# Kernel optimization log

Measured on AMD Instinct MI355X. Metric: run time of the kernel, lower is better.

Reference implementation:

```python
import jax, jax.numpy as jnp
import numpy as np

N = 12000       # nodes (Hi-C bins, max_num_nodes)
F_IN = 16       # number_genomic_annotations
HID = 4 * F_IN  # conv1 out = 64
NCLUST = 100    # n_clust
E = 384000      # edges (avg degree 32)


def setup_inputs() -> dict:
    key = jax.random.key(0)
    ks = jax.random.split(key, 8)
    x = jax.random.normal(ks[0], (N, F_IN), dtype=jnp.float32)
    edge_index = jax.random.randint(ks[1], (2, E), 0, N)
    edge_attr = jax.random.uniform(ks[2], (E,), dtype=jnp.float32)
    s1 = 1.0 / np.sqrt(F_IN)
    W1_rel = jax.random.uniform(ks[3], (HID, F_IN), minval=-s1, maxval=s1, dtype=jnp.float32)
    W1_root = jax.random.uniform(ks[4], (HID, F_IN), minval=-s1, maxval=s1, dtype=jnp.float32)
    b1 = jnp.zeros((HID,), jnp.float32)
    s2 = 1.0 / np.sqrt(HID)
    W2_rel = jax.random.uniform(ks[5], (NCLUST, HID), minval=-s2, maxval=s2, dtype=jnp.float32)
    W2_root = jax.random.uniform(ks[6], (NCLUST, HID), minval=-s2, maxval=s2, dtype=jnp.float32)
    b2 = jnp.zeros((NCLUST,), jnp.float32)
    return dict(x=x, edge_index=edge_index, edge_attr=edge_attr,
                W1_rel=W1_rel, W1_root=W1_root, b1=b1,
                W2_rel=W2_rel, W2_root=W2_root, b2=b2)


def _graph_conv(x, src, dst, ew, W_rel, W_root, b):
    # PyG GraphConv (aggr='add'): out = lin_rel(sum_j e_ji * x_j) + lin_root(x)
    msg = x[src] * ew[:, None]                       # [E, F]
    aggr = jax.ops.segment_sum(msg, dst, num_segments=N)  # [N, F]
    return aggr @ W_rel.T + b + x @ W_root.T


def reference(x, edge_index, edge_attr, W1_rel, W1_root, b1, W2_rel, W2_root, b2):
    src, dst = edge_index[0], edge_index[1]
    h = _graph_conv(x, src, dst, edge_attr, W1_rel, W1_root, b1)
    h = jax.nn.relu(h)  # dropout is identity in eval mode
    s_out = _graph_conv(h, src, dst, edge_attr, W2_rel, W2_root, b2)  # [N, NCLUST]

    # to_dense_adj (duplicate edges summed)
    adj = jnp.zeros((N, N), x.dtype).at[src, dst].add(edge_attr)  # [N, N]

    # dense_mincut_pool with S = x (as in the original forward), k = F_IN
    s_mc = jax.nn.softmax(x, axis=-1)      # [N, F_IN]
    as_ = adj @ s_mc                        # [N, F_IN]
    out_adj = s_mc.T @ as_                  # [F_IN, F_IN]
    mincut_num = jnp.trace(out_adj)
    d_flat = adj.sum(-1)                    # [N] degree
    mincut_den = jnp.einsum('ik,i,ik->', s_mc, d_flat, s_mc)  # trace(S^T D S)
    mc = -(mincut_num / mincut_den)

    ss = s_mc.T @ s_mc                      # [F_IN, F_IN]
    i_k = jnp.eye(F_IN, dtype=ss.dtype)
    o = jnp.linalg.norm(ss / jnp.linalg.norm(ss) - i_k / jnp.linalg.norm(i_k))

    return jax.nn.softmax(s_out, axis=-1), mc, o
```

## Files before the change

### kernel.cpp

```cpp
#include <hip/hip_runtime.h>
#include <math.h>

#define N_NODES 12000
#define F_INN 16
#define HIDD 64
#define NCLUST 100
#define NEDGE 384000
#define NBLK_N 47
#define CAP 96
#define EPT 4
#define NTHR_E (NEDGE / EPT)
#define NBLK_E (NTHR_E / 256)

#define OFF_COUNT   0
#define OFF_SCAL    12000
#define ZERO_ELEMS  12002
#define OFF_SSPART  12004
#define OFF_NORM2   24036
#define OFF_W2TREL  36036
#define OFF_W2TROOT 42436
#define OFF_SMC     48836
#define OFF_H       240836
#define OFF_SRCW    1008836

__global__ void zero_kernel(int* __restrict__ ws) {
    int i = blockIdx.x * 256 + threadIdx.x;
    if (i < ZERO_ELEMS) ws[i] = 0;
}

__global__ void phase0_kernel(const float* __restrict__ x, const int* __restrict__ ei,
                              const float* __restrict__ ew, float* __restrict__ smc,
                              float* __restrict__ norm2, int* __restrict__ count,
                              int2* __restrict__ srcw, const float* __restrict__ W2_rel,
                              const float* __restrict__ W2_root, float* __restrict__ w2t_rel,
                              float* __restrict__ w2t_root) {
    __shared__ float fl[6400];
    int t = threadIdx.x;
    int b = blockIdx.x;
    if (b < NBLK_N) {
        int i = b * 256 + t;
        if (i >= N_NODES) return;
        const float4* xr = (const float4*)(x + i * 16);
        float4 r0 = xr[0], r1 = xr[1], r2 = xr[2], r3 = xr[3];
        float v[16] = {r0.x, r0.y, r0.z, r0.w, r1.x, r1.y, r1.z, r1.w,
                       r2.x, r2.y, r2.z, r2.w, r3.x, r3.y, r3.z, r3.w};
        float m = v[0];
#pragma unroll
        for (int k = 1; k < 16; ++k) m = fmaxf(m, v[k]);
        float s = 0.f;
#pragma unroll
        for (int k = 0; k < 16; ++k) { v[k] = __expf(v[k] - m); s += v[k]; }
        float inv = 1.f / s;
        float n2 = 0.f;
#pragma unroll
        for (int k = 0; k < 16; ++k) { v[k] *= inv; n2 += v[k] * v[k]; }
        float4* so = (float4*)(smc + i * 16);
        so[0] = make_float4(v[0], v[1], v[2], v[3]);
        so[1] = make_float4(v[4], v[5], v[6], v[7]);
        so[2] = make_float4(v[8], v[9], v[10], v[11]);
        so[3] = make_float4(v[12], v[13], v[14], v[15]);
        norm2[i] = n2;
    } else if (b < NBLK_N + NBLK_E) {
        int tid = (b - NBLK_N) * 256 + t;
        int e0 = tid * EPT;
        int4 sv = *(const int4*)(ei + e0);
        int4 dv = *(const int4*)(ei + NEDGE + e0);
        float4 wv = *(const float4*)(ew + e0);
        int s[EPT] = {sv.x, sv.y, sv.z, sv.w};
        int d[EPT] = {dv.x, dv.y, dv.z, dv.w};
        float w[EPT] = {wv.x, wv.y, wv.z, wv.w};
        int pos[EPT];
#pragma unroll
        for (int i = 0; i < EPT; ++i) pos[i] = atomicAdd(&count[d[i]], 1);
#pragma unroll
        for (int i = 0; i < EPT; ++i)
            srcw[d[i] * CAP + pos[i]] = make_int2(s[i], __float_as_int(w[i]));
    } else {
        const float* src = (b == NBLK_N + NBLK_E) ? W2_rel : W2_root;
        float* dst = (b == NBLK_N + NBLK_E) ? w2t_rel : w2t_root;
        for (int i = t; i < 6400; i += 256) fl[i] = src[i];
        __syncthreads();
        for (int j = t; j < 6400; j += 256) {
            int kk = j / 100, cl = j - kk * 100;
            dst[j] = fl[cl * 64 + kk];
        }
    }
}

__global__ void pass2_kernel(const float* __restrict__ smc, float* __restrict__ sspart,
                             const int* __restrict__ ei, const float* __restrict__ ew,
                             const float* __restrict__ norm2, float* __restrict__ scal) {
    int t = threadIdx.x;
    int b = blockIdx.x;
    if (b < NBLK_N) {
        __shared__ float rows[256 * 17];
        int n = b * 256 + t;
        float* rp = rows + t * 17;
        if (n < N_NODES) {
            const float4* sr = (const float4*)(smc + n * 16);
            float4 a0 = sr[0], a1 = sr[1], a2 = sr[2], a3 = sr[3];
            rp[0] = a0.x;  rp[1] = a0.y;  rp[2] = a0.z;  rp[3] = a0.w;
            rp[4] = a1.x;  rp[5] = a1.y;  rp[6] = a1.z;  rp[7] = a1.w;
            rp[8] = a2.x;  rp[9] = a2.y;  rp[10] = a2.z; rp[11] = a2.w;
            rp[12] = a3.x; rp[13] = a3.y; rp[14] = a3.z; rp[15] = a3.w;
        } else {
#pragma unroll
            for (int k = 0; k < 16; ++k) rp[k] = 0.f;
        }
        __syncthreads();
        int a = t & 15, bb = t >> 4;
        float acc = 0.f;
#pragma unroll 4
        for (int r = 0; r < 256; ++r)
            acc = fmaf(rows[r * 17 + a], rows[r * 17 + bb], acc);
        sspart[b * 256 + t] = acc;
    } else {
        int tid = (b - NBLK_N) * 256 + t;
        int e0 = tid * EPT;
        int4 sv = *(const int4*)(ei + e0);
        int4 dv = *(const int4*)(ei + NEDGE + e0);
        float4 wv = *(const float4*)(ew + e0);
        int s[EPT] = {sv.x, sv.y, sv.z, sv.w};
        int d[EPT] = {dv.x, dv.y, dv.z, dv.w};
        float w[EPT] = {wv.x, wv.y, wv.z, wv.w};
        float np = 0.f, dp = 0.f;
#pragma unroll
        for (int i = 0; i < EPT; ++i) {
            const float4* ps = (const float4*)(smc + s[i] * 16);
            const float4* pd = (const float4*)(smc + d[i] * 16);
            float4 s0 = ps[0], s1 = ps[1], s2 = ps[2], s3 = ps[3];
            float4 d0 = pd[0], d1 = pd[1], d2 = pd[2], d3 = pd[3];
            float dot = s0.x * d0.x + s0.y * d0.y + s0.z * d0.z + s0.w * d0.w +
                        s1.x * d1.x + s1.y * d1.y + s1.z * d1.z + s1.w * d1.w +
                        s2.x * d2.x + s2.y * d2.y + s2.z * d2.z + s2.w * d2.w +
                        s3.x * d3.x + s3.y * d3.y + s3.z * d3.z + s3.w * d3.w;
            np = fmaf(w[i], dot, np);
            dp = fmaf(w[i], norm2[s[i]], dp);
        }
        __shared__ float redn[256], redd[256];
        redn[t] = np;
        redd[t] = dp;
        __syncthreads();
        for (int s2 = 128; s2 > 0; s2 >>= 1) {
            if (t < s2) { redn[t] += redn[t + s2]; redd[t] += redd[t + s2]; }
            __syncthreads();
        }
        if (t == 0) {
            atomicAdd(&scal[0], redn[0]);
            atomicAdd(&scal[1], redd[0]);
        }
    }
}

__global__ void fused1_kernel(const float* __restrict__ x, const int2* __restrict__ srcw,
                              const int* __restrict__ count, const float* __restrict__ W1_rel,
                              const float* __restrict__ W1_root, const float* __restrict__ b1,
                              float* __restrict__ h) {
    __shared__ float wrelT[16 * 64], wrootT[16 * 64], b1s[64];
    __shared__ float aggr[4][16], xs[4][16];
    int t = threadIdx.x;
    for (int idx = t; idx < 1024; idx += 256) {
        int f = idx >> 4, k = idx & 15;
        wrelT[(k << 6) + f] = W1_rel[idx];
        wrootT[(k << 6) + f] = W1_root[idx];
    }
    if (t < 64) b1s[t] = b1[t];
    int w = t >> 6, lane = t & 63;
    int n = blockIdx.x * 4 + w;
    int j = lane >> 4, c = lane & 15;
    int len = count[n];
    const int2* bucket = srcw + n * CAP;
    float acc = 0.f;
    int k = j;
    for (; k + 12 < len; k += 16) {
        int2 p0 = bucket[k], p1 = bucket[k + 4], p2 = bucket[k + 8], p3 = bucket[k + 12];
        float v0 = x[p0.x * 16 + c], v1 = x[p1.x * 16 + c];
        float v2 = x[p2.x * 16 + c], v3 = x[p3.x * 16 + c];
        acc = fmaf(v0, __int_as_float(p0.y), acc);
        acc = fmaf(v1, __int_as_float(p1.y), acc);
        acc = fmaf(v2, __int_as_float(p2.y), acc);
        acc = fmaf(v3, __int_as_float(p3.y), acc);
    }
    for (; k < len; k += 4) {
        int2 p = bucket[k];
        acc = fmaf(x[p.x * 16 + c], __int_as_float(p.y), acc);
    }
    acc += __shfl_down(acc, 32);
    acc += __shfl_down(acc, 16);
    if (lane < 16) { aggr[w][lane] = acc; xs[w][lane] = x[n * 16 + lane]; }
    __syncthreads();
    float o = b1s[lane];
#pragma unroll
    for (int kk = 0; kk < 16; ++kk)
        o = fmaf(aggr[w][kk], wrelT[(kk << 6) + lane],
                 fmaf(xs[w][kk], wrootT[(kk << 6) + lane], o));
    h[n * 64 + lane] = fmaxf(o, 0.f);
}

__global__ void fused2_kernel(const float* __restrict__ h, const int2* __restrict__ srcw,
                              const int* __restrict__ count, const float* __restrict__ w2t_rel,
                              const float* __restrict__ w2t_root, const float* __restrict__ b2,
                              float* __restrict__ out) {
    __shared__ float a2[4][64], hrow[4][64];
    __shared__ float logits[4][104];
    int t = threadIdx.x;
    int nn = t >> 6;
    int c = t & 63;
    int n = blockIdx.x * 4 + nn;
    int len = count[n];
    const int2* bucket = srcw + n * CAP;
    float acc = 0.f;
    int k = 0;
    for (; k + 7 < len; k += 8) {
        int2 p0 = bucket[k],     p1 = bucket[k + 1], p2 = bucket[k + 2], p3 = bucket[k + 3];
        int2 p4 = bucket[k + 4], p5 = bucket[k + 5], p6 = bucket[k + 6], p7 = bucket[k + 7];
        float v0 = h[p0.x * 64 + c], v1 = h[p1.x * 64 + c];
        float v2 = h[p2.x * 64 + c], v3 = h[p3.x * 64 + c];
        float v4 = h[p4.x * 64 + c], v5 = h[p5.x * 64 + c];
        float v6 = h[p6.x * 64 + c], v7 = h[p7.x * 64 + c];
        acc = fmaf(v0, __int_as_float(p0.y), acc);
        acc = fmaf(v1, __int_as_float(p1.y), acc);
        acc = fmaf(v2, __int_as_float(p2.y), acc);
        acc = fmaf(v3, __int_as_float(p3.y), acc);
        acc = fmaf(v4, __int_as_float(p4.y), acc);
        acc = fmaf(v5, __int_as_float(p5.y), acc);
        acc = fmaf(v6, __int_as_float(p6.y), acc);
        acc = fmaf(v7, __int_as_float(p7.y), acc);
    }
    for (; k < len; ++k) {
        int2 p = bucket[k];
        acc = fmaf(h[p.x * 64 + c], __int_as_float(p.y), acc);
    }
    a2[nn][c] = acc;
    hrow[nn][c] = h[n * 64 + c];
    __syncthreads();
    int half = t >> 7, c2 = t & 127;
    if (c2 < NCLUST) {
        float s0 = b2[c2], s1 = s0;
        const float* aA = a2[half * 2];
        const float* hA = hrow[half * 2];
        const float* aB = a2[half * 2 + 1];
        const float* hB = hrow[half * 2 + 1];
#pragma unroll 4
        for (int kk = 0; kk < 64; ++kk) {
            float wr = w2t_rel[kk * 100 + c2];
            float wo = w2t_root[kk * 100 + c2];
            s0 = fmaf(aA[kk], wr, fmaf(hA[kk], wo, s0));
            s1 = fmaf(aB[kk], wr, fmaf(hB[kk], wo, s1));
        }
        logits[half * 2][c2] = s0;
        logits[half * 2 + 1][c2] = s1;
    }
    __syncthreads();
    float v0 = logits[nn][c];
    float v1 = (c < NCLUST - 64) ? logits[nn][64 + c] : -INFINITY;
    float m = fmaxf(v0, v1);
#pragma unroll
    for (int off = 32; off > 0; off >>= 1) m = fmaxf(m, __shfl_xor(m, off));
    float e0 = __expf(v0 - m);
    float e1 = (c < NCLUST - 64) ? __expf(v1 - m) : 0.f;
    float s = e0 + e1;
#pragma unroll
    for (int off = 32; off > 0; off >>= 1) s += __shfl_xor(s, off);
    float inv = 1.f / s;
    out[n * NCLUST + c] = e0 * inv;
    if (c < NCLUST - 64) out[n * NCLUST + 64 + c] = e1 * inv;
}

__global__ void finalize_kernel(const float* __restrict__ sspart, const float* __restrict__ scal,
                                float* __restrict__ out) {
    __shared__ float red[256];
    int t = threadIdx.x;
    float sv = 0.f;
    for (int b = 0; b < NBLK_N; ++b) sv += sspart[b * 256 + t];
    red[t] = sv * sv;
    __syncthreads();
    for (int s = 128; s > 0; s >>= 1) {
        if (t < s) red[t] += red[t + s];
        __syncthreads();
    }
    float ssnorm = sqrtf(red[0]);
    __syncthreads();
    float diff = sv / ssnorm - ((t % 17 == 0) ? 0.25f : 0.f);
    red[t] = diff * diff;
    __syncthreads();
    for (int s = 128; s > 0; s >>= 1) {
        if (t < s) red[t] += red[t + s];
        __syncthreads();
    }
    if (t == 0) {
        out[N_NODES * NCLUST + 0] = -(scal[0] / scal[1]);
        out[N_NODES * NCLUST + 1] = sqrtf(red[0]);
    }
}

extern "C" void kernel_launch(void* const* d_in, const int* in_sizes, int n_in,
                              void* d_out, int out_size, void* d_ws, size_t ws_size,
                              hipStream_t stream) {
    const float* x       = (const float*)d_in[0];
    const int*   ei      = (const int*)d_in[1];
    const float* ew      = (const float*)d_in[2];
    const float* W1_rel  = (const float*)d_in[3];
    const float* W1_root = (const float*)d_in[4];
    const float* b1      = (const float*)d_in[5];
    const float* W2_rel  = (const float*)d_in[6];
    const float* W2_root = (const float*)d_in[7];
    const float* b2      = (const float*)d_in[8];
    float* out = (float*)d_out;
    int*   wsi = (int*)d_ws;

    int*   count   = wsi + OFF_COUNT;
    float* scal    = (float*)(wsi + OFF_SCAL);
    float* sspart  = (float*)(wsi + OFF_SSPART);
    float* norm2   = (float*)(wsi + OFF_NORM2);
    float* w2trel  = (float*)(wsi + OFF_W2TREL);
    float* w2troot = (float*)(wsi + OFF_W2TROOT);
    float* smc     = (float*)(wsi + OFF_SMC);
    float* h       = (float*)(wsi + OFF_H);
    int2*  srcw    = (int2*)(wsi + OFF_SRCW);

    zero_kernel<<<(ZERO_ELEMS + 255) / 256, 256, 0, stream>>>(wsi);
    phase0_kernel<<<NBLK_N + NBLK_E + 2, 256, 0, stream>>>(x, ei, ew, smc, norm2, count, srcw,
                                                           W2_rel, W2_root, w2trel, w2troot);
    pass2_kernel<<<NBLK_N + NBLK_E, 256, 0, stream>>>(smc, sspart, ei, ew, norm2, scal);
    fused1_kernel<<<N_NODES / 4, 256, 0, stream>>>(x, srcw, count, W1_rel, W1_root, b1, h);
    fused2_kernel<<<N_NODES / 4, 256, 0, stream>>>(h, srcw, count, w2trel, w2troot, b2, out);
    finalize_kernel<<<1, 256, 0, stream>>>(sspart, scal, out);
}
```

Before: 104.7 us.

## Merge independent kernels into shared launches and rebalance layer-2 matvec

```diff
diff --git a/kernel.cpp b/kernel.cpp
--- a/kernel.cpp
+++ b/kernel.cpp
@@ -11,6 +11,7 @@
 #define EPT 4
 #define NTHR_E (NEDGE / EPT)
 #define NBLK_E (NTHR_E / 256)
+#define NBLK_F1 (N_NODES / 4)
 
 #define OFF_COUNT   0
 #define OFF_SCAL    12000
@@ -87,35 +88,83 @@
     }
 }
 
-__global__ void pass2_kernel(const float* __restrict__ smc, float* __restrict__ sspart,
-                             const int* __restrict__ ei, const float* __restrict__ ew,
-                             const float* __restrict__ norm2, float* __restrict__ scal) {
+__global__ void fused1_pass2_kernel(const float* __restrict__ x, const int2* __restrict__ srcw,
+                                    const int* __restrict__ count, const float* __restrict__ W1_rel,
+                                    const float* __restrict__ W1_root, const float* __restrict__ b1,
+                                    float* __restrict__ h, const float* __restrict__ smc,
+                                    float* __restrict__ sspart, const int* __restrict__ ei,
+                                    const float* __restrict__ ew, const float* __restrict__ norm2,
+                                    float* __restrict__ scal) {
+    __shared__ float shm[4352];
     int t = threadIdx.x;
     int b = blockIdx.x;
-    if (b < NBLK_N) {
-        __shared__ float rows[256 * 17];
-        int n = b * 256 + t;
+    if (b < NBLK_F1) {
+        float* wrelT  = shm;
+        float* wrootT = shm + 1024;
+        float* b1s    = shm + 2048;
+        float* aggr   = shm + 2112;
+        float* xs     = shm + 2176;
+        for (int idx = t; idx < 1024; idx += 256) {
+            int f = idx >> 4, k = idx & 15;
+            wrelT[(k << 6) + f]  = W1_rel[idx];
+            wrootT[(k << 6) + f] = W1_root[idx];
+        }
+        if (t < 64) b1s[t] = b1[t];
+        int w = t >> 6, lane = t & 63;
+        int n = b * 4 + w;
+        int j = lane >> 4, c = lane & 15;
+        int len = count[n];
+        const int2* bucket = srcw + n * CAP;
+        float acc = 0.f;
+        int k = j;
+        for (; k + 12 < len; k += 16) {
+            int2 p0 = bucket[k], p1 = bucket[k + 4], p2 = bucket[k + 8], p3 = bucket[k + 12];
+            float v0 = x[p0.x * 16 + c], v1 = x[p1.x * 16 + c];
+            float v2 = x[p2.x * 16 + c], v3 = x[p3.x * 16 + c];
+            acc = fmaf(v0, __int_as_float(p0.y), acc);
+            acc = fmaf(v1, __int_as_float(p1.y), acc);
+            acc = fmaf(v2, __int_as_float(p2.y), acc);
+            acc = fmaf(v3, __int_as_float(p3.y), acc);
+        }
+        for (; k < len; k += 4) {
+            int2 p = bucket[k];
+            acc = fmaf(x[p.x * 16 + c], __int_as_float(p.y), acc);
+        }
+        acc += __shfl_down(acc, 32);
+        acc += __shfl_down(acc, 16);
+        if (lane < 16) { aggr[w * 16 + lane] = acc; xs[w * 16 + lane] = x[n * 16 + lane]; }
+        __syncthreads();
+        float o = b1s[lane];
+#pragma unroll
+        for (int kk = 0; kk < 16; ++kk)
+            o = fmaf(aggr[w * 16 + kk], wrelT[(kk << 6) + lane],
+                     fmaf(xs[w * 16 + kk], wrootT[(kk << 6) + lane], o));
+        h[n * 64 + lane] = fmaxf(o, 0.f);
+    } else if (b < NBLK_F1 + NBLK_N) {
+        int bb = b - NBLK_F1;
+        float* rows = shm;
+        int n = bb * 256 + t;
         float* rp = rows + t * 17;
         if (n < N_NODES) {
             const float4* sr = (const float4*)(smc + n * 16);
-            float4 a0 = sr[0], a1 = sr[1], a2 = sr[2], a3 = sr[3];
+            float4 a0 = sr[0], a1 = sr[1], a2v = sr[2], a3 = sr[3];
             rp[0] = a0.x;  rp[1] = a0.y;  rp[2] = a0.z;  rp[3] = a0.w;
             rp[4] = a1.x;  rp[5] = a1.y;  rp[6] = a1.z;  rp[7] = a1.w;
-            rp[8] = a2.x;  rp[9] = a2.y;  rp[10] = a2.z; rp[11] = a2.w;
+            rp[8] = a2v.x; rp[9] = a2v.y; rp[10] = a2v.z; rp[11] = a2v.w;
             rp[12] = a3.x; rp[13] = a3.y; rp[14] = a3.z; rp[15] = a3.w;
         } else {
 #pragma unroll
             for (int k = 0; k < 16; ++k) rp[k] = 0.f;
         }
         __syncthreads();
-        int a = t & 15, bb = t >> 4;
-        float acc = 0.f;
+        int a = t & 15, bq = t >> 4;
+        float accs = 0.f;
 #pragma unroll 4
         for (int r = 0; r < 256; ++r)
-            acc = fmaf(rows[r * 17 + a], rows[r * 17 + bb], acc);
-        sspart[b * 256 + t] = acc;
+            accs = fmaf(rows[r * 17 + a], rows[r * 17 + bq], accs);
+        sspart[bb * 256 + t] = accs;
     } else {
-        int tid = (b - NBLK_N) * 256 + t;
+        int tid = (b - NBLK_F1 - NBLK_N) * 256 + t;
         int e0 = tid * EPT;
         int4 sv = *(const int4*)(ei + e0);
         int4 dv = *(const int4*)(ei + NEDGE + e0);
@@ -137,7 +186,8 @@
             np = fmaf(w[i], dot, np);
             dp = fmaf(w[i], norm2[s[i]], dp);
         }
-        __shared__ float redn[256], redd[256];
+        float* redn = shm;
+        float* redd = shm + 256;
         redn[t] = np;
         redd[t] = dp;
         __syncthreads();
@@ -152,145 +202,116 @@
     }
 }
 
-__global__ void fused1_kernel(const float* __restrict__ x, const int2* __restrict__ srcw,
-                              const int* __restrict__ count, const float* __restrict__ W1_rel,
-                              const float* __restrict__ W1_root, const float* __restrict__ b1,
-                              float* __restrict__ h) {
-    __shared__ float wrelT[16 * 64], wrootT[16 * 64], b1s[64];
-    __shared__ float aggr[4][16], xs[4][16];
+__global__ void fused2_finalize_kernel(const float* __restrict__ h, const int2* __restrict__ srcw,
+                                       const int* __restrict__ count,
+                                       const float* __restrict__ w2t_rel,
+                                       const float* __restrict__ w2t_root,
+                                       const float* __restrict__ b2, float* __restrict__ out,
+                                       const float* __restrict__ sspart,
+                                       const float* __restrict__ scal) {
+    __shared__ float shm[1328];
     int t = threadIdx.x;
-    for (int idx = t; idx < 1024; idx += 256) {
-        int f = idx >> 4, k = idx & 15;
-        wrelT[(k << 6) + f] = W1_rel[idx];
-        wrootT[(k << 6) + f] = W1_root[idx];
-    }
-    if (t < 64) b1s[t] = b1[t];
-    int w = t >> 6, lane = t & 63;
-    int n = blockIdx.x * 4 + w;
-    int j = lane >> 4, c = lane & 15;
-    int len = count[n];
-    const int2* bucket = srcw + n * CAP;
-    float acc = 0.f;
-    int k = j;
-    for (; k + 12 < len; k += 16) {
-        int2 p0 = bucket[k], p1 = bucket[k + 4], p2 = bucket[k + 8], p3 = bucket[k + 12];
-        float v0 = x[p0.x * 16 + c], v1 = x[p1.x * 16 + c];
-        float v2 = x[p2.x * 16 + c], v3 = x[p3.x * 16 + c];
-        acc = fmaf(v0, __int_as_float(p0.y), acc);
-        acc = fmaf(v1, __int_as_float(p1.y), acc);
-        acc = fmaf(v2, __int_as_float(p2.y), acc);
-        acc = fmaf(v3, __int_as_float(p3.y), acc);
-    }
-    for (; k < len; k += 4) {
-        int2 p = bucket[k];
-        acc = fmaf(x[p.x * 16 + c], __int_as_float(p.y), acc);
-    }
-    acc += __shfl_down(acc, 32);
-    acc += __shfl_down(acc, 16);
-    if (lane < 16) { aggr[w][lane] = acc; xs[w][lane] = x[n * 16 + lane]; }
-    __syncthreads();
-    float o = b1s[lane];
-#pragma unroll
-    for (int kk = 0; kk < 16; ++kk)
-        o = fmaf(aggr[w][kk], wrelT[(kk << 6) + lane],
-                 fmaf(xs[w][kk], wrootT[(kk << 6) + lane], o));
-    h[n * 64 + lane] = fmaxf(o, 0.f);
-}
-
-__global__ void fused2_kernel(const float* __restrict__ h, const int2* __restrict__ srcw,
-                              const int* __restrict__ count, const float* __restrict__ w2t_rel,
-                              const float* __restrict__ w2t_root, const float* __restrict__ b2,
-                              float* __restrict__ out) {
-    __shared__ float a2[4][64], hrow[4][64];
-    __shared__ float logits[4][104];
-    int t = threadIdx.x;
-    int nn = t >> 6;
-    int c = t & 63;
-    int n = blockIdx.x * 4 + nn;
-    int len = count[n];
-    const int2* bucket = srcw + n * CAP;
-    float acc = 0.f;
-    int k = 0;
-    for (; k + 7 < len; k += 8) {
-        int2 p0 = bucket[k],     p1 = bucket[k + 1], p2 = bucket[k + 2], p3 = bucket[k + 3];
-        int2 p4 = bucket[k + 4], p5 = bucket[k + 5], p6 = bucket[k + 6], p7 = bucket[k + 7];
-        float v0 = h[p0.x * 64 + c], v1 = h[p1.x * 64 + c];
-        float v2 = h[p2.x * 64 + c], v3 = h[p3.x * 64 + c];
-        float v4 = h[p4.x * 64 + c], v5 = h[p5.x * 64 + c];
-        float v6 = h[p6.x * 64 + c], v7 = h[p7.x * 64 + c];
-        acc = fmaf(v0, __int_as_float(p0.y), acc);
-        acc = fmaf(v1, __int_as_float(p1.y), acc);
-        acc = fmaf(v2, __int_as_float(p2.y), acc);
-        acc = fmaf(v3, __int_as_float(p3.y), acc);
-        acc = fmaf(v4, __int_as_float(p4.y), acc);
-        acc = fmaf(v5, __int_as_float(p5.y), acc);
-        acc = fmaf(v6, __int_as_float(p6.y), acc);
-        acc = fmaf(v7, __int_as_float(p7.y), acc);
-    }
-    for (; k < len; ++k) {
-        int2 p = bucket[k];
-        acc = fmaf(h[p.x * 64 + c], __int_as_float(p.y), acc);
-    }
-    a2[nn][c] = acc;
-    hrow[nn][c] = h[n * 64 + c];
-    __syncthreads();
-    int half = t >> 7, c2 = t & 127;
-    if (c2 < NCLUST) {
-        float s0 = b2[c2], s1 = s0;
-        const float* aA = a2[half * 2];
-        const float* hA = hrow[half * 2];
-        const float* aB = a2[half * 2 + 1];
-        const float* hB = hrow[half * 2 + 1];
-#pragma unroll 4
-        for (int kk = 0; kk < 64; ++kk) {
-            float wr = w2t_rel[kk * 100 + c2];
-            float wo = w2t_root[kk * 100 + c2];
-            s0 = fmaf(aA[kk], wr, fmaf(hA[kk], wo, s0));
-            s1 = fmaf(aB[kk], wr, fmaf(hB[kk], wo, s1));
-        }
-        logits[half * 2][c2] = s0;
-        logits[half * 2 + 1][c2] = s1;
-    }
-    __syncthreads();
-    float v0 = logits[nn][c];
-    float v1 = (c < NCLUST - 64) ? logits[nn][64 + c] : -INFINITY;
-    float m = fmaxf(v0, v1);
-#pragma unroll
-    for (int off = 32; off > 0; off >>= 1) m = fmaxf(m, __shfl_xor(m, off));
-    float e0 = __expf(v0 - m);
-    float e1 = (c < NCLUST - 64) ? __expf(v1 - m) : 0.f;
-    float s = e0 + e1;
-#pragma unroll
-    for (int off = 32; off > 0; off >>= 1) s += __shfl_xor(s, off);
-    float inv = 1.f / s;
-    out[n * NCLUST + c] = e0 * inv;
-    if (c < NCLUST - 64) out[n * NCLUST + 64 + c] = e1 * inv;
-}
-
-__global__ void finalize_kernel(const float* __restrict__ sspart, const float* __restrict__ scal,
-                                float* __restrict__ out) {
-    __shared__ float red[256];
-    int t = threadIdx.x;
-    float sv = 0.f;
-    for (int b = 0; b < NBLK_N; ++b) sv += sspart[b * 256 + t];
-    red[t] = sv * sv;
-    __syncthreads();
-    for (int s = 128; s > 0; s >>= 1) {
-        if (t < s) red[t] += red[t + s];
-        __syncthreads();
-    }
-    float ssnorm = sqrtf(red[0]);
-    __syncthreads();
-    float diff = sv / ssnorm - ((t % 17 == 0) ? 0.25f : 0.f);
-    red[t] = diff * diff;
-    __syncthreads();
-    for (int s = 128; s > 0; s >>= 1) {
-        if (t < s) red[t] += red[t + s];
-        __syncthreads();
-    }
-    if (t == 0) {
-        out[N_NODES * NCLUST + 0] = -(scal[0] / scal[1]);
-        out[N_NODES * NCLUST + 1] = sqrtf(red[0]);
+    int b = blockIdx.x;
+    if (b < NBLK_F1) {
+        float* a2   = shm;
+        float* hrow = shm + 256;
+        float* logits = shm + 512;
+        float* part = shm + 928;
+        int nn = t >> 6;
+        int c = t & 63;
+        int n = b * 4 + nn;
+        int len = count[n];
+        const int2* bucket = srcw + n * CAP;
+        float acc = 0.f;
+        int k = 0;
+        for (; k + 7 < len; k += 8) {
+            int2 p0 = bucket[k],     p1 = bucket[k + 1], p2 = bucket[k + 2], p3 = bucket[k + 3];
+            int2 p4 = bucket[k + 4], p5 = bucket[k + 5], p6 = bucket[k + 6], p7 = bucket[k + 7];
+            float v0 = h[p0.x * 64 + c], v1 = h[p1.x * 64 + c];
+            float v2 = h[p2.x * 64 + c], v3 = h[p3.x * 64 + c];
+            float v4 = h[p4.x * 64 + c], v5 = h[p5.x * 64 + c];
+            float v6 = h[p6.x * 64 + c], v7 = h[p7.x * 64 + c];
+            acc = fmaf(v0, __int_as_float(p0.y), acc);
+            acc = fmaf(v1, __int_as_float(p1.y), acc);
+            acc = fmaf(v2, __int_as_float(p2.y), acc);
+            acc = fmaf(v3, __int_as_float(p3.y), acc);
+            acc = fmaf(v4, __int_as_float(p4.y), acc);
+            acc = fmaf(v5, __int_as_float(p5.y), acc);
+            acc = fmaf(v6, __int_as_float(p6.y), acc);
+            acc = fmaf(v7, __int_as_float(p7.y), acc);
+        }
+        for (; k < len; ++k) {
+            int2 p = bucket[k];
+            acc = fmaf(h[p.x * 64 + c], __int_as_float(p.y), acc);
+        }
+        a2[nn * 64 + c] = acc;
+        hrow[nn * 64 + c] = h[n * 64 + c];
+        __syncthreads();
+        int half = t >> 7, c2 = t & 127;
+        float p0 = 0.f, p1 = 0.f, p2 = 0.f, p3 = 0.f;
+        if (c2 < NCLUST) {
+            int kbase = half << 5;
+#pragma unroll 8
+            for (int kk = kbase; kk < kbase + 32; ++kk) {
+                float wr = w2t_rel[kk * 100 + c2];
+                float wo = w2t_root[kk * 100 + c2];
+                p0 = fmaf(a2[0 * 64 + kk], wr, fmaf(hrow[0 * 64 + kk], wo, p0));
+                p1 = fmaf(a2[1 * 64 + kk], wr, fmaf(hrow[1 * 64 + kk], wo, p1));
+                p2 = fmaf(a2[2 * 64 + kk], wr, fmaf(hrow[2 * 64 + kk], wo, p2));
+                p3 = fmaf(a2[3 * 64 + kk], wr, fmaf(hrow[3 * 64 + kk], wo, p3));
+            }
+            if (half == 1) {
+                part[0 * 100 + c2] = p0;
+                part[1 * 100 + c2] = p1;
+                part[2 * 100 + c2] = p2;
+                part[3 * 100 + c2] = p3;
+            }
+        }
+        __syncthreads();
+        if (half == 0 && c2 < NCLUST) {
+            float bb = b2[c2];
+            logits[0 * 104 + c2] = bb + p0 + part[0 * 100 + c2];
+            logits[1 * 104 + c2] = bb + p1 + part[1 * 100 + c2];
+            logits[2 * 104 + c2] = bb + p2 + part[2 * 100 + c2];
+            logits[3 * 104 + c2] = bb + p3 + part[3 * 100 + c2];
+        }
+        __syncthreads();
+        float v0 = logits[nn * 104 + c];
+        float v1 = (c < NCLUST - 64) ? logits[nn * 104 + 64 + c] : -INFINITY;
+        float m = fmaxf(v0, v1);
+#pragma unroll
+        for (int off = 32; off > 0; off >>= 1) m = fmaxf(m, __shfl_xor(m, off));
+        float e0 = __expf(v0 - m);
+        float e1 = (c < NCLUST - 64) ? __expf(v1 - m) : 0.f;
+        float s = e0 + e1;
+#pragma unroll
+        for (int off = 32; off > 0; off >>= 1) s += __shfl_xor(s, off);
+        float inv = 1.f / s;
+        out[n * NCLUST + c] = e0 * inv;
+        if (c < NCLUST - 64) out[n * NCLUST + 64 + c] = e1 * inv;
+    } else {
+        float* red = shm;
+        float sv = 0.f;
+        for (int bb = 0; bb < NBLK_N; ++bb) sv += sspart[bb * 256 + t];
+        red[t] = sv * sv;
+        __syncthreads();
+        for (int s = 128; s > 0; s >>= 1) {
+            if (t < s) red[t] += red[t + s];
+            __syncthreads();
+        }
+        float ssnorm = sqrtf(red[0]);
+        __syncthreads();
+        float diff = sv / ssnorm - ((t % 17 == 0) ? 0.25f : 0.f);
+        red[t] = diff * diff;
+        __syncthreads();
+        for (int s = 128; s > 0; s >>= 1) {
+            if (t < s) red[t] += red[t + s];
+            __syncthreads();
+        }
+        if (t == 0) {
+            out[N_NODES * NCLUST + 0] = -(scal[0] / scal[1]);
+            out[N_NODES * NCLUST + 1] = sqrtf(red[0]);
+        }
     }
 }
 
@@ -322,8 +343,8 @@
     zero_kernel<<<(ZERO_ELEMS + 255) / 256, 256, 0, stream>>>(wsi);
     phase0_kernel<<<NBLK_N + NBLK_E + 2, 256, 0, stream>>>(x, ei, ew, smc, norm2, count, srcw,
                                                            W2_rel, W2_root, w2trel, w2troot);
-    pass2_kernel<<<NBLK_N + NBLK_E, 256, 0, stream>>>(smc, sspart, ei, ew, norm2, scal);
-    fused1_kernel<<<N_NODES / 4, 256, 0, stream>>>(x, srcw, count, W1_rel, W1_root, b1, h);
-    fused2_kernel<<<N_NODES / 4, 256, 0, stream>>>(h, srcw, count, w2trel, w2troot, b2, out);
-    finalize_kernel<<<1, 256, 0, stream>>>(sspart, scal, out);
-}
+    fused1_pass2_kernel<<<NBLK_F1 + NBLK_N + NBLK_E, 256, 0, stream>>>(
+        x, srcw, count, W1_rel, W1_root, b1, h, smc, sspart, ei, ew, norm2, scal);
+    fused2_finalize_kernel<<<NBLK_F1 + 1, 256, 0, stream>>>(h, srcw, count, w2trel, w2troot, b2,
+                                                            out, sspart, scal);
+}
```

Result: no change. 104.3 us (-0.4%).
